# Performance work log

Hardware: AMD Instinct MI355X
Metric: run time of the kernel (lower is better)

Reference implementation:

```python
import jax, jax.numpy as jnp
import numpy as np

B, C, N, D = 8, 4, 1024, 96
H, DK, DV = 3, 32, 32
EPS = 1e-5


def setup_inputs() -> dict:
    key = jax.random.key(0)
    ks = jax.random.split(key, 7)
    s = 1.0 / np.sqrt(D)
    return {
        "input_Q": jax.random.normal(ks[0], (B, C, N, D), jnp.float32),
        "input_K": jax.random.normal(ks[1], (B, C, N, D), jnp.float32),
        "input_V": jax.random.normal(ks[2], (B, C, N, D), jnp.float32),
        "W_Q": jax.random.normal(ks[3], (H * DK, D), jnp.float32) * s,
        "W_K": jax.random.normal(ks[4], (H * DK, D), jnp.float32) * s,
        "W_V": jax.random.normal(ks[5], (H * DV, D), jnp.float32) * s,
        "W_fc": jax.random.normal(ks[6], (D, H * DV), jnp.float32) * s,
        "ln_gamma": jnp.ones((D,), jnp.float32),
        "ln_beta": jnp.zeros((D,), jnp.float32),
    }


def reference(input_Q, input_K, input_V, W_Q, W_K, W_V, W_fc, ln_gamma, ln_beta):
    # projections (torch Linear: x @ W.T), then split heads: [B,C,N,H*dk] -> [B,C,H,N,dk]
    def split_heads(x, W, dh):
        y = jnp.einsum('bcnd,ed->bcne', x, W)
        return y.reshape(B, C, N, H, dh).transpose(0, 1, 3, 2, 4)

    Q = split_heads(input_Q, W_Q, DK)
    K = split_heads(input_K, W_K, DK)
    V = split_heads(input_V, W_V, DV)

    scores = jnp.einsum('bchqd,bchkd->bchqk', Q, K) / np.sqrt(DK).astype(np.float32)
    # NOTE: original code softmaxes over dim=3 of the 5D scores == the QUERY axis
    attn = jax.nn.softmax(scores, axis=3)
    context = jnp.einsum('bchqk,bchkd->bchqd', attn, V)
    context = context.transpose(0, 1, 3, 2, 4).reshape(B, C, N, H * DV)

    out = jnp.einsum('bcne,de->bcnd', context, W_fc) + input_Q  # residual
    mu = jnp.mean(out, axis=-1, keepdims=True)
    var = jnp.var(out, axis=-1, keepdims=True)
    return (out - mu) * jax.lax.rsqrt(var + EPS) * ln_gamma + ln_beta
```

## Files before the change

### kernel.cpp

```cpp
#include <hip/hip_runtime.h>
#include <hip/hip_bf16.h>

#define NB 8
#define NC 4
#define NN 1024
#define ND 96
#define NHH 3
#define DKV 32
#define NBC (NB*NC)
#define NHEAD (NBC*NHH)
#define NROWS (NBC*NN)
#define C1 0.25503486910638953f
#define EPSV 1e-5f

using short8 = __attribute__((ext_vector_type(8))) short;
using sh4    = __attribute__((ext_vector_type(4))) short;
using f32x4  = __attribute__((ext_vector_type(4))) float;
using f32x16 = __attribute__((ext_vector_type(16))) float;

__device__ __forceinline__ short bf16_of(float f) {
  __hip_bfloat16 h = __float2bfloat16(f);
  return __builtin_bit_cast(short, h);
}
__device__ __forceinline__ float f_of_bf16(short s) {
  return __bfloat162float(__builtin_bit_cast(__hip_bfloat16, s));
}

__device__ __forceinline__ short8 load_cvt8(const float* p) {
  float4 f0 = *(const float4*)p;
  float4 f1 = *(const float4*)(p + 4);
  short8 v;
  v[0] = bf16_of(f0.x); v[1] = bf16_of(f0.y); v[2] = bf16_of(f0.z); v[3] = bf16_of(f0.w);
  v[4] = bf16_of(f1.x); v[5] = bf16_of(f1.y); v[6] = bf16_of(f1.z); v[7] = bf16_of(f1.w);
  return v;
}

__device__ __forceinline__ void gload_lds16(const void* g, void* l) {
  __builtin_amdgcn_global_load_lds(
      (const __attribute__((address_space(1))) unsigned int*)g,
      (__attribute__((address_space(3))) unsigned int*)l,
      16, 0, 0);
}

__global__ __launch_bounds__(256) void proj_kernel(
    const float* __restrict__ xq, const float* __restrict__ xk, const float* __restrict__ xv,
    const float* __restrict__ Wq, const float* __restrict__ Wk, const float* __restrict__ Wv,
    short* __restrict__ qb, short* __restrict__ kb, short* __restrict__ vb)
{
  __shared__ __align__(16) short wlds[96][104];
  __shared__ __align__(16) short xlds[64][104];
  const int t = threadIdx.x;
  const int p = blockIdx.x >> 9;
  const int blkrow0 = (blockIdx.x & 511) * 64;

  const float* x = (p == 0) ? xq : (p == 1) ? xk : xv;
  const float* W = (p == 0) ? Wq : (p == 1) ? Wk : Wv;
  short* dst = (p == 0) ? qb : (p == 1) ? kb : vb;
  const float sc = (p == 1) ? C1 : 1.0f;

  for (int idx = t; idx < 96*96; idx += 256)
    wlds[idx/96][idx%96] = bf16_of(W[idx]);
#pragma unroll
  for (int it = 0; it < 3; ++it) {
    const int f = it*2048 + t*8;
    const int row = f / 96, col = f % 96;
    *(short8*)&xlds[row][col] = load_cvt8(x + (size_t)(blkrow0 + row)*ND + col);
  }
  __syncthreads();

  const int wave = t >> 6, lane = t & 63;
  const int g = lane >> 4, li = lane & 15;
  const int acol = g * 8;

  const short8 a0 = *(const short8*)&xlds[wave*16 + li][acol];
  const short8 a1 = *(const short8*)&xlds[wave*16 + li][32 + acol];
  const short8 a2 = *(const short8*)&xlds[wave*16 + li][64 + acol];

  f32x4 oacc[6];
#pragma unroll
  for (int tt = 0; tt < 6; ++tt) {
    f32x4 acc = {0.f, 0.f, 0.f, 0.f};
    const short* wr = &wlds[tt*16 + li][acol];
    acc = __builtin_amdgcn_mfma_f32_16x16x32_bf16(a0, *(const short8*)(wr),      acc, 0, 0, 0);
    acc = __builtin_amdgcn_mfma_f32_16x16x32_bf16(a1, *(const short8*)(wr + 32), acc, 0, 0, 0);
    acc = __builtin_amdgcn_mfma_f32_16x16x32_bf16(a2, *(const short8*)(wr + 64), acc, 0, 0, 0);
    oacc[tt] = acc;
  }

#pragma unroll
  for (int tt = 0; tt < 6; ++tt)
#pragma unroll
    for (int r = 0; r < 4; ++r)
      xlds[wave*16 + g*4 + r][tt*16 + li] = bf16_of(oacc[tt][r] * sc);
  __syncthreads();

#pragma unroll
  for (int it = 0; it < 3; ++it) {
    const int task = it*256 + t;
    const int nn_l = task / 12, seg = task - nn_l*12;
    const int col8 = seg*8;
    const int h = col8 >> 5, dd = col8 & 31;
    const int n = blkrow0 + nn_l;
    const int bcx = n >> 10, nnx = n & 1023;
    *(short8*)&dst[((size_t)(bcx*NHH + h)*NN + nnx)*DKV + dd] =
        *(const short8*)&xlds[nn_l][col8];
  }
}

__global__ __launch_bounds__(256) void stats_kernel(
    const short* __restrict__ qb, const short* __restrict__ kb,
    const short* __restrict__ vb, short* __restrict__ vtb)
{
  __shared__ __align__(16) short s_q[2][128][40];
  __shared__ float s_is[128];
  __shared__ __align__(16) short s_t[32][128];

  const int t = threadIdx.x, wave = t >> 6, lane = t & 63;
  const int g = lane >> 4, li = lane & 15;
  const int head = blockIdx.x % NHEAD;
  const int kblk = blockIdx.x / NHEAD;
  const int kb0 = kblk*128;
  const int k0 = kb0 + wave*32;

  const short* kr = kb + ((size_t)head*NN + k0)*DKV + g*8;
  const short8 af0 = *(const short8*)(kr + (size_t)li*DKV);
  const short8 af1 = *(const short8*)(kr + (size_t)(16 + li)*DKV);

  const int nl = t >> 1;
  const int dvs = (t & 1) * 16;
  const short* vrow = vb + ((size_t)head*NN + kb0 + nl)*DKV + dvs;
  const short8 v0 = *(const short8*)(vrow);
  const short8 v1 = *(const short8*)(vrow + 8);

  const short* qhead = qb + (size_t)head*NN*DKV;
  const int srow = t >> 1;
  const int sseg = (t & 1) * 16;

  f32x4 s0 = {0.f,0.f,0.f,0.f}, s1 = {0.f,0.f,0.f,0.f};

  *(short8*)&s_q[0][srow][sseg]     = *(const short8*)(qhead + (size_t)srow*DKV + sseg);
  *(short8*)&s_q[0][srow][sseg + 8] = *(const short8*)(qhead + (size_t)srow*DKV + sseg + 8);
  __syncthreads();

  for (int qc = 0; qc < 8; ++qc) {
    const int cur = qc & 1;
    short8 nxt0, nxt1;
    if (qc < 7) {
      nxt0 = *(const short8*)(qhead + (size_t)((qc+1)*128 + srow)*DKV + sseg);
      nxt1 = *(const short8*)(qhead + (size_t)((qc+1)*128 + srow)*DKV + sseg + 8);
    }
    __builtin_amdgcn_s_setprio(1);
#pragma unroll
    for (int qt = 0; qt < 8; ++qt) {
      const short8 bf = *(const short8*)&s_q[cur][qt*16 + li][g*8];
      f32x4 z = {0.f,0.f,0.f,0.f};
      f32x4 d0 = __builtin_amdgcn_mfma_f32_16x16x32_bf16(af0, bf, z, 0, 0, 0);
      f32x4 d1 = __builtin_amdgcn_mfma_f32_16x16x32_bf16(af1, bf, z, 0, 0, 0);
#pragma unroll
      for (int r = 0; r < 4; ++r) {
        s0[r] += __builtin_amdgcn_exp2f(d0[r]);
        s1[r] += __builtin_amdgcn_exp2f(d1[r]);
      }
    }
    __builtin_amdgcn_s_setprio(0);
    if (qc < 7) {
      *(short8*)&s_q[cur^1][srow][sseg]     = nxt0;
      *(short8*)&s_q[cur^1][srow][sseg + 8] = nxt1;
    }
    __syncthreads();
  }

#pragma unroll
  for (int ms = 1; ms <= 8; ms <<= 1) {
#pragma unroll
    for (int r = 0; r < 4; ++r) {
      s0[r] += __shfl_xor(s0[r], ms);
      s1[r] += __shfl_xor(s1[r], ms);
    }
  }
  if (li == 0) {
    float* dst = s_is + wave*32 + g*4;
#pragma unroll
    for (int r = 0; r < 4; ++r) {
      dst[r]      = 1.0f / s0[r];
      dst[16 + r] = 1.0f / s1[r];
    }
  }
  __syncthreads();

  {
    const float isv = s_is[nl];
    short* st = &s_t[0][0];
#pragma unroll
    for (int j = 0; j < 8; ++j) {
      const int dv0 = dvs + j, dv1 = dvs + 8 + j;
      st[dv0*128 + (((nl*2) ^ ((dv0 & 7) << 4)) >> 1)] = bf16_of(isv * f_of_bf16(v0[j]));
      st[dv1*128 + (((nl*2) ^ ((dv1 & 7) << 4)) >> 1)] = bf16_of(isv * f_of_bf16(v1[j]));
    }
  }
  __syncthreads();

  {
    const short* st = &s_t[0][0];
#pragma unroll
    for (int it = 0; it < 2; ++it) {
      const int task = it*256 + t;
      const int dv = task >> 4, ns = task & 15;
      short8 v = *(const short8*)(st + dv*128 + (((ns*16) ^ ((dv & 7) << 4)) >> 1));
      *(short8*)(vtb + ((size_t)head*DKV + dv)*NN + kb0 + ns*8) = v;
    }
  }
}

__global__ __launch_bounds__(384) void ctxout_kernel(
    const short* __restrict__ qb, const short* __restrict__ kb,
    const short* __restrict__ vtb, const float* __restrict__ resid,
    const float* __restrict__ Wfc, const float* __restrict__ gamma,
    const float* __restrict__ beta, float* __restrict__ out)
{
  __shared__ __align__(16) char smem[49152];

  const int t = threadIdx.x;
  const int w = t >> 6, lane = t & 63;
  const int li = lane & 31, hi = lane >> 5;
  const int hs = t >> 7;
  const int sub = w & 1;
  const int bc = blockIdx.x % NBC;
  const int qtile = blockIdx.x / NBC;
  const int q0 = qtile*64 + sub*32;
  const int head = bc*NHH + hs;

  float4 wreg[6];
#pragma unroll
  for (int i = 0; i < 6; ++i)
    wreg[i] = *(const float4*)(Wfc + i*1536 + t*4);

  char* kbase = smem + hs*16384;
  char* vbase = kbase + 8192;

  const short* kgp = kb  + (size_t)head*NN*DKV;
  const short* vgp = vtb + (size_t)head*DKV*NN;
  const short* qrow = qb + ((size_t)head*NN + q0 + li)*DKV;
  const short8 qf0 = *(const short8*)(qrow + hi*8);
  const short8 qf1 = *(const short8*)(qrow + 16 + hi*8);

  int kgoff[2], vgoff[2], ldsseg[2];
#pragma unroll
  for (int j = 0; j < 2; ++j) {
    const int b = (sub*2 + j)*1024 + lane*16;
    const int r = b >> 7, c = b & 127;
    const int pc = c ^ ((r & 7) << 4);
    const int xk6 = r + 32*(pc >> 6);
    const int kr = (xk6 & 51) | ((xk6 & 4) << 1) | ((xk6 & 8) >> 1);
    kgoff[j] = kr*64 + (pc & 63);
    vgoff[j] = r*(NN*2) + pc;
    ldsseg[j] = (sub*2 + j)*1024;
  }

  int rd_off[2][2];
#pragma unroll
  for (int kt = 0; kt < 2; ++kt) {
    const int base = kt*64 + hi*16;
    rd_off[kt][0] = li*128 + ((base)      ^ ((li & 7) << 4));
    rd_off[kt][1] = li*128 + ((base + 32) ^ ((li & 7) << 4));
  }

  f32x16 acc = {0.f,0.f,0.f,0.f,0.f,0.f,0.f,0.f,0.f,0.f,0.f,0.f,0.f,0.f,0.f,0.f};

#pragma unroll
  for (int j = 0; j < 2; ++j) {
    gload_lds16((const char*)kgp + kgoff[j], kbase + ldsseg[j]);
    gload_lds16((const char*)vgp + vgoff[j], vbase + ldsseg[j]);
  }
  __syncthreads();

  for (int kc = 0; kc < 16; ++kc) {
    const int cur = kc & 1;
    if (kc < 15) {
      const size_t kadv = (size_t)(kc+1)*4096;
      const int vadv = (kc+1)*128;
#pragma unroll
      for (int j = 0; j < 2; ++j) {
        gload_lds16((const char*)kgp + kadv + kgoff[j],
                    kbase + (cur^1)*4096 + ldsseg[j]);
        gload_lds16((const char*)vgp + vadv + vgoff[j],
                    vbase + (cur^1)*4096 + ldsseg[j]);
      }
    }
    const char* kc_b = kbase + cur*4096;
    const char* vc_b = vbase + cur*4096;

    __builtin_amdgcn_s_setprio(1);
#pragma unroll
    for (int kt = 0; kt < 2; ++kt) {
      const short8 a0 = *(const short8*)(kc_b + rd_off[kt][0]);
      const short8 a1 = *(const short8*)(kc_b + rd_off[kt][1]);
      f32x16 sT = {0.f,0.f,0.f,0.f,0.f,0.f,0.f,0.f,0.f,0.f,0.f,0.f,0.f,0.f,0.f,0.f};
      sT = __builtin_amdgcn_mfma_f32_32x32x16_bf16(a0, qf0, sT, 0, 0, 0);
      sT = __builtin_amdgcn_mfma_f32_32x32x16_bf16(a1, qf1, sT, 0, 0, 0);
      short8 pa0, pa1;
#pragma unroll
      for (int j = 0; j < 8; ++j) {
        pa0[j] = bf16_of(__builtin_amdgcn_exp2f(sT[j]));
        pa1[j] = bf16_of(__builtin_amdgcn_exp2f(sT[8 + j]));
      }
      const short8 vfa = *(const short8*)(vc_b + rd_off[kt][0]);
      const short8 vfb = *(const short8*)(vc_b + rd_off[kt][1]);
      acc = __builtin_amdgcn_mfma_f32_32x32x16_bf16(pa0, vfa, acc, 0, 0, 0);
      acc = __builtin_amdgcn_mfma_f32_32x32x16_bf16(pa1, vfb, acc, 0, 0, 0);
    }
    __builtin_amdgcn_s_setprio(0);

    __syncthreads();
  }

  short* s_ct = (short*)smem;
  short* wlds = (short*)(smem + 13312);

#pragma unroll
  for (int reg = 0; reg < 16; ++reg) {
    const int ql = sub*32 + (reg & 3) + 8*(reg >> 2) + 4*hi;
    s_ct[ql*104 + hs*32 + li] = bf16_of(acc[reg]);
  }
#pragma unroll
  for (int i = 0; i < 6; ++i) {
    const int f = i*1536 + t*4;
    const int row = f / 96, col = f % 96;
    sh4 w4;
    w4[0] = bf16_of(wreg[i].x); w4[1] = bf16_of(wreg[i].y);
    w4[2] = bf16_of(wreg[i].z); w4[3] = bf16_of(wreg[i].w);
    *(sh4*)&wlds[row*104 + col] = w4;
  }
  __syncthreads();

  if (w < 4) {
    const int g16 = lane >> 4, li16 = lane & 15;
    const int rbase = w*16;
    const size_t rowg = (size_t)bc*NN + qtile*64 + rbase;

    const short* ar = s_ct + (rbase + li16)*104 + g16*8;
    const short8 a0 = *(const short8*)(ar);
    const short8 a1 = *(const short8*)(ar + 32);
    const short8 a2 = *(const short8*)(ar + 64);

    float o[6][4];
#pragma unroll
    for (int tt = 0; tt < 6; ++tt) {
      f32x4 oa = {0.f, 0.f, 0.f, 0.f};
      const short* wr = wlds + (tt*16 + li16)*104 + g16*8;
      oa = __builtin_amdgcn_mfma_f32_16x16x32_bf16(a0, *(const short8*)(wr),      oa, 0, 0, 0);
      oa = __builtin_amdgcn_mfma_f32_16x16x32_bf16(a1, *(const short8*)(wr + 32), oa, 0, 0, 0);
      oa = __builtin_amdgcn_mfma_f32_16x16x32_bf16(a2, *(const short8*)(wr + 64), oa, 0, 0, 0);
#pragma unroll
      for (int r = 0; r < 4; ++r)
        o[tt][r] = oa[r] + resid[(rowg + g16*4 + r)*ND + tt*16 + li16];
    }

    float s1v[4], s2v[4];
#pragma unroll
    for (int r = 0; r < 4; ++r) {
      float a = 0.f, b = 0.f;
#pragma unroll
      for (int tt = 0; tt < 6; ++tt) { a += o[tt][r]; b += o[tt][r]*o[tt][r]; }
      s1v[r] = a; s2v[r] = b;
    }
#pragma unroll
    for (int ms = 1; ms <= 8; ms <<= 1) {
#pragma unroll
      for (int r = 0; r < 4; ++r) {
        s1v[r] += __shfl_xor(s1v[r], ms);
        s2v[r] += __shfl_xor(s2v[r], ms);
      }
    }
    float mean[4], rs[4];
#pragma unroll
    for (int r = 0; r < 4; ++r) {
      mean[r] = s1v[r] * (1.0f/96.0f);
      float var = s2v[r]*(1.0f/96.0f) - mean[r]*mean[r];
      rs[r] = rsqrtf(var + EPSV);
    }
#pragma unroll
    for (int tt = 0; tt < 6; ++tt) {
      const int e = tt*16 + li16;
      const float gg = gamma[e], bb = beta[e];
#pragma unroll
      for (int r = 0; r < 4; ++r)
        out[(rowg + g16*4 + r)*ND + e] = (o[tt][r] - mean[r])*rs[r]*gg + bb;
    }
  }
}

extern "C" void kernel_launch(void* const* d_in, const int* in_sizes, int n_in,
                              void* d_out, int out_size, void* d_ws, size_t ws_size,
                              hipStream_t stream) {
  (void)in_sizes; (void)n_in; (void)out_size; (void)ws_size;
  const float* xq    = (const float*)d_in[0];
  const float* xk    = (const float*)d_in[1];
  const float* xv    = (const float*)d_in[2];
  const float* Wq    = (const float*)d_in[3];
  const float* Wk    = (const float*)d_in[4];
  const float* Wv    = (const float*)d_in[5];
  const float* Wfc   = (const float*)d_in[6];
  const float* gamma = (const float*)d_in[7];
  const float* beta  = (const float*)d_in[8];
  float* out = (float*)d_out;

  short* qb  = (short*)d_ws;
  short* kb  = qb  + (size_t)NHEAD*NN*DKV;
  short* vtb = kb  + (size_t)NHEAD*NN*DKV;
  short* vb  = vtb + (size_t)NHEAD*NN*DKV;

  hipLaunchKernelGGL(proj_kernel,   dim3(3*NROWS/64), dim3(256), 0, stream,
                     xq, xk, xv, Wq, Wk, Wv, qb, kb, vb);
  hipLaunchKernelGGL(stats_kernel,  dim3(NHEAD*8), dim3(256), 0, stream,
                     qb, kb, vb, vtb);
  hipLaunchKernelGGL(ctxout_kernel, dim3(NBC*16), dim3(384), 0, stream,
                     qb, kb, vtb, xq, Wfc, gamma, beta, out);
}
```

Before: 58.28 us.

## Use direct global-to-LDS loads for Q chunks and vectorize weight staging

In the stats kernel, Q chunks are now streamed straight from global memory into a flat, unpadded LDS double buffer with gload_lds16. This replaces the register round-trip and the explicit LDS store after the MFMA loop. The projection kernel now loads weights as float4 and converts them in groups of four instead of one scalar at a time. Dropping the row padding in the Q buffer may add LDS bank conflicts on the MFMA operand reads. The async load also depends on the barrier to order correctly with the double buffer.

After: 56.58 us, median of 2. 1.03x faster.

```diff
diff --git a/kernel.cpp b/kernel.cpp
--- a/kernel.cpp
+++ b/kernel.cpp
@@ -58,8 +58,16 @@
   short* dst = (p == 0) ? qb : (p == 1) ? kb : vb;
   const float sc = (p == 1) ? C1 : 1.0f;
 
-  for (int idx = t; idx < 96*96; idx += 256)
-    wlds[idx/96][idx%96] = bf16_of(W[idx]);
+#pragma unroll
+  for (int i = 0; i < 9; ++i) {
+    const int idx = i*256 + t;
+    const float4 wv = *(const float4*)(W + (size_t)idx*4);
+    const int f = idx*4, row = f/96, col = f%96;
+    sh4 w4;
+    w4[0] = bf16_of(wv.x); w4[1] = bf16_of(wv.y);
+    w4[2] = bf16_of(wv.z); w4[3] = bf16_of(wv.w);
+    *(sh4*)&wlds[row][col] = w4;
+  }
 #pragma unroll
   for (int it = 0; it < 3; ++it) {
     const int f = it*2048 + t*8;
@@ -111,7 +119,7 @@
     const short* __restrict__ qb, const short* __restrict__ kb,
     const short* __restrict__ vb, short* __restrict__ vtb)
 {
-  __shared__ __align__(16) short s_q[2][128][40];
+  __shared__ __align__(16) short s_q[2][4096];
   __shared__ float s_is[128];
   __shared__ __align__(16) short s_t[32][128];
 
@@ -132,27 +140,32 @@
   const short8 v0 = *(const short8*)(vrow);
   const short8 v1 = *(const short8*)(vrow + 8);
 
-  const short* qhead = qb + (size_t)head*NN*DKV;
-  const int srow = t >> 1;
-  const int sseg = (t & 1) * 16;
+  const char* qsrc = (const char*)(qb + (size_t)head*NN*DKV);
+  char* sq0 = (char*)&s_q[0][0];
+  char* sq1 = (char*)&s_q[1][0];
+  const int wseg = wave*2048;
 
   f32x4 s0 = {0.f,0.f,0.f,0.f}, s1 = {0.f,0.f,0.f,0.f};
 
-  *(short8*)&s_q[0][srow][sseg]     = *(const short8*)(qhead + (size_t)srow*DKV + sseg);
-  *(short8*)&s_q[0][srow][sseg + 8] = *(const short8*)(qhead + (size_t)srow*DKV + sseg + 8);
+#pragma unroll
+  for (int j = 0; j < 2; ++j)
+    gload_lds16(qsrc + wseg + j*1024 + lane*16, sq0 + wseg + j*1024);
   __syncthreads();
 
   for (int qc = 0; qc < 8; ++qc) {
     const int cur = qc & 1;
-    short8 nxt0, nxt1;
+    const short* scur = (const short*)(cur ? sq1 : sq0);
+    char* snxt = cur ? sq0 : sq1;
     if (qc < 7) {
-      nxt0 = *(const short8*)(qhead + (size_t)((qc+1)*128 + srow)*DKV + sseg);
-      nxt1 = *(const short8*)(qhead + (size_t)((qc+1)*128 + srow)*DKV + sseg + 8);
+#pragma unroll
+      for (int j = 0; j < 2; ++j)
+        gload_lds16(qsrc + (size_t)(qc+1)*8192 + wseg + j*1024 + lane*16,
+                    snxt + wseg + j*1024);
     }
     __builtin_amdgcn_s_setprio(1);
 #pragma unroll
     for (int qt = 0; qt < 8; ++qt) {
-      const short8 bf = *(const short8*)&s_q[cur][qt*16 + li][g*8];
+      const short8 bf = *(const short8*)(scur + (qt*16 + li)*32 + g*8);
       f32x4 z = {0.f,0.f,0.f,0.f};
       f32x4 d0 = __builtin_amdgcn_mfma_f32_16x16x32_bf16(af0, bf, z, 0, 0, 0);
       f32x4 d1 = __builtin_amdgcn_mfma_f32_16x16x32_bf16(af1, bf, z, 0, 0, 0);
@@ -163,10 +176,6 @@
       }
     }
     __builtin_amdgcn_s_setprio(0);
-    if (qc < 7) {
-      *(short8*)&s_q[cur^1][srow][sseg]     = nxt0;
-      *(short8*)&s_q[cur^1][srow][sseg + 8] = nxt1;
-    }
     __syncthreads();
   }
 
```
